# Performance work log

Hardware: AMD Instinct MI355X
Metric: run time of the kernel (lower is better)

The kernel has to match this reference:

```python
import jax, jax.numpy as jnp
import numpy as np
import math

_EPS = 1e-5          # _SAMPLING_EPS
_K_PER_CHUNK = 32    # _TOPK_K_PER_CHUNK
_MAX_CHUNK = 32768   # _TOPK_MAX_CHUNK_SIZE
B, V = 128, 128256


def setup_inputs() -> dict:
    key = jax.random.key(0)
    ks = jax.random.split(key, 10)
    logits = jax.random.normal(ks[0], (B, V), dtype=jnp.float32) * 4.0
    temperature = jax.random.uniform(ks[1], (B,), dtype=jnp.float32) * 1.5
    top_k = jax.random.randint(ks[2], (B,), 0, 100)  # 0 => top-k disabled
    top_p = 0.5 + 0.5 * jax.random.uniform(ks[3], (B,), dtype=jnp.float32)
    output_token_counts = jax.random.randint(ks[4], (B, V), 0, 3).astype(jnp.float32)
    prompt_token_mask = jax.random.randint(ks[5], (B, V), 0, 2).astype(bool)
    presence_penalties = jax.random.uniform(ks[6], (B,), dtype=jnp.float32)
    frequency_penalties = jax.random.uniform(ks[7], (B,), dtype=jnp.float32)
    repetition_penalties = 1.0 + 0.5 * jax.random.uniform(ks[8], (B,), dtype=jnp.float32)
    u = jax.random.uniform(ks[9], (B, V), dtype=jnp.float32, minval=1e-6, maxval=1.0)
    q_samples = -jnp.log(u)  # Exponential(1) noise, vLLM random_sample convention
    return dict(logits=logits, temperature=temperature, top_k=top_k, top_p=top_p,
                output_token_counts=output_token_counts, prompt_token_mask=prompt_token_mask,
                presence_penalties=presence_penalties, frequency_penalties=frequency_penalties,
                repetition_penalties=repetition_penalties, q_samples=q_samples)


def _apply_penalties(logits, counts, prompt_mask, presence, frequency, repetition):
    counts = counts.astype(logits.dtype)
    prompt_f = prompt_mask.astype(logits.dtype)
    occurred = counts - jnp.maximum(counts - 1.0, 0.0)            # 1 if count>0 else 0
    rep_union = occurred + prompt_f
    rep_mask = rep_union - jnp.maximum(rep_union - 1.0, 0.0)      # 1 if in prompt or output
    rep = repetition[:, None]
    pos = jnp.maximum(logits, 0.0)
    neg = jnp.minimum(logits, 0.0)
    penalized = pos / rep + neg * rep
    logits = logits + rep_mask * (penalized - logits)
    logits = logits - frequency[:, None] * counts - presence[:, None] * occurred
    return logits


def _chunked_topk(logits):
    # split vocab into <=32768 chunks, top-32 per chunk (multi-core ttnn.topk emulation)
    b, v = logits.shape
    num_chunks = math.ceil(v / _MAX_CHUNK)
    chunk_size = math.ceil(v / num_chunks)
    pad = num_chunks * chunk_size - v
    x = jnp.pad(logits, ((0, 0), (0, pad)), constant_values=-np.inf) if pad else logits
    x = x.reshape(b, num_chunks, chunk_size)
    vals, inds = jax.lax.top_k(x, _K_PER_CHUNK)                   # [b, nc, k]
    inds = inds + (jnp.arange(num_chunks, dtype=inds.dtype) * chunk_size)[None, :, None]
    return vals.reshape(b, -1), inds.reshape(b, -1)               # [b, nc*k]


def _filter_topk_topp(all_values, k, p, vocab_size):
    C = all_values.shape[-1]
    probs = jax.nn.softmax(all_values, axis=-1)
    probs_sort = jnp.sort(probs, axis=-1)                         # ascending
    # top-k on candidate set
    count_k = jnp.clip(C - k.astype(jnp.int32), 0, C - 1)[:, None]
    cutoff_k = jnp.take_along_axis(probs_sort, count_k, axis=-1)
    no_k = ((k <= 0) | (k >= vocab_size))[:, None]
    cutoff_k = jnp.where(no_k, -np.inf, cutoff_k)
    all_values = jnp.where(probs < cutoff_k, -np.inf, all_values)
    # top-p on candidate set
    cumprob = jnp.cumsum(probs_sort, axis=-1)
    mask = cumprob <= (1.0 - p)[:, None]
    mask = mask.at[:, -1].set(False)
    count_p = jnp.sum(mask, axis=-1, dtype=jnp.int32)[:, None]
    cutoff_p = jnp.take_along_axis(probs_sort, count_p, axis=-1)
    all_values = jnp.where(probs < cutoff_p, -np.inf, all_values)
    return all_values


def reference(logits, temperature, top_k, top_p, output_token_counts, prompt_token_mask,
              presence_penalties, frequency_penalties, repetition_penalties, q_samples):
    logits = logits.astype(jnp.float32)
    logits = _apply_penalties(logits, output_token_counts, prompt_token_mask,
                              presence_penalties, frequency_penalties, repetition_penalties)
    greedy = jnp.argmax(logits, axis=-1)                          # [B]
    temp_eff = jnp.where(temperature < _EPS, 1.0, temperature)
    logits_t = logits / temp_eff[:, None]
    vals, inds = _chunked_topk(logits_t)                          # [B, 128] each
    filtered = _filter_topk_topp(vals, top_k, top_p, logits.shape[-1])
    probs = jax.nn.softmax(filtered, axis=-1)                     # fp32 softmax on candidates
    q_red = jnp.take_along_axis(q_samples, inds, axis=1)
    local = jnp.argmax(probs / q_red, axis=-1)                    # exponential-noise sampling
    random_sampled = jnp.take_along_axis(inds, local[:, None], axis=1)[:, 0]
    sampled = jnp.where(temperature < _EPS, greedy, random_sampled.astype(greedy.dtype))
    return sampled[:, None], probs                                # sampled_token_ids [B,1]
```

## Files before the change

kernel.cpp:

```cpp
#include <hip/hip_runtime.h>
#include <math.h>

#define BATCH   128
#define VOCAB   128256
#define NCHUNK  4
#define CSIZE   32064
#define CVEC    (CSIZE / 4)
#define T1      1024
#define NBKT    2048
#define CAP     2048
#define KSEL    32
#define CWIDTH  (NCHUNK * KSEL)
#define T2      128
#define TAILTID 848

__device__ __forceinline__ unsigned fenc(float f) {
    unsigned u = __float_as_uint(f);
    return (u & 0x80000000u) ? ~u : (u | 0x80000000u);
}

__device__ __forceinline__ float penalize(float l, float cnt, float pf,
                                          float rep, float freq, float pres) {
    float occ   = __fsub_rn(cnt, fmaxf(__fsub_rn(cnt, 1.0f), 0.0f));
    float ru    = __fadd_rn(occ, pf);
    float rmask = __fsub_rn(ru, fmaxf(__fsub_rn(ru, 1.0f), 0.0f));
    float pos   = fmaxf(l, 0.0f);
    float neg   = fminf(l, 0.0f);
    float pen   = __fadd_rn(__fdiv_rn(pos, rep), __fmul_rn(neg, rep));
    float p     = __fadd_rn(l, __fmul_rn(rmask, __fsub_rn(pen, l)));
    p = __fsub_rn(p, __fmul_rn(freq, cnt));
    p = __fsub_rn(p, __fmul_rn(pres, occ));
    return p;
}

__device__ __forceinline__ unsigned ldmask(const void* pm, long base, int i, int mtype) {
    if (mtype == 0) {
        return ((const unsigned*)((const unsigned char*)pm + base))[i];
    } else if (mtype == 1) {
        int4 m = ((const int4*)((const int*)pm + base))[i];
        return (m.x ? 1u : 0u) | (m.y ? 0x100u : 0u) | (m.z ? 0x10000u : 0u) | (m.w ? 0x1000000u : 0u);
    } else {
        float4 f = ((const float4*)((const float*)pm + base))[i];
        return ((f.x != 0.f) ? 1u : 0u) | ((f.y != 0.f) ? 0x100u : 0u) |
               ((f.z != 0.f) ? 0x10000u : 0u) | ((f.w != 0.f) ? 0x1000000u : 0u);
    }
}

__global__ __launch_bounds__(T1, 4) void sampler_k1(
    const float* __restrict__ logits, const float* __restrict__ counts,
    const void* __restrict__ pmask,
    const float* __restrict__ temperature, const float* __restrict__ presence,
    const float* __restrict__ frequency, const float* __restrict__ repetition,
    float* __restrict__ g_topv, int* __restrict__ g_topi,
    float* __restrict__ g_gval, int* __restrict__ g_gidx)
{
    const int b   = blockIdx.x >> 2;
    const int c   = blockIdx.x & 3;
    const int tid = threadIdx.x;
    const long base = (long)b * VOCAB + (long)c * CSIZE;

    __shared__ unsigned hist[NBKT];
    __shared__ float    cv[CAP];
    __shared__ int      ci[CAP];
    __shared__ unsigned ccnt;
    __shared__ int      s_tb;
    __shared__ int      s_m0, s_mf;
    __shared__ float    wrv[16];
    __shared__ int      wri[16];

    for (int i = tid; i < NBKT; i += T1) hist[i] = 0;
    if (tid == 0) { ccnt = 0; s_m0 = 1; s_mf = 1; }
    __syncthreads();

    {
        const unsigned* w = (const unsigned*)pmask;
        int a01 = 1, af = 1;
        for (int i = tid; i < 4096; i += T1) {
            unsigned x = w[i];
            if (!(x == 0u || x == 1u)) a01 = 0;
            if (!(x == 0u || x == 0x3F800000u)) af = 0;
        }
        if (!a01) atomicAnd(&s_m0, 0);
        if (!af)  atomicAnd(&s_mf, 0);
    }
    __syncthreads();
    const int mtype = s_m0 ? 1 : (s_mf ? 2 : 0);

    const float temp = temperature[b];
    const float teff = (temp < 1e-5f) ? 1.0f : temp;
    const float pres = presence[b];
    const float freq = frequency[b];
    const float rep  = repetition[b];

    const float4* l4 = (const float4*)(logits + base);
    const float4* c4 = (const float4*)(counts + base);

    float gmax = -INFINITY;
    int   gidx = 0x7fffffff;

    const bool tail = tid < TAILTID;

    float4 v0, v1, v2, v3, v4, v5, v6, v7;
    v7.x = v7.y = v7.z = v7.w = 0.0f;

#define PROC1(Lv, Cv, Mv, Vv, I0) do {                                          \
        float p_;                                                               \
        p_ = penalize((Lv).x, (Cv).x, ((Mv) & 0x000000ffu) ? 1.0f : 0.0f,       \
                      rep, freq, pres);                                         \
        if (p_ > gmax) { gmax = p_; gidx = (I0) * 4 + 0; }                      \
        (Vv).x = __fdiv_rn(p_, teff);                                           \
        atomicAdd(&hist[fenc((Vv).x) >> 21], 1u);                               \
        p_ = penalize((Lv).y, (Cv).y, ((Mv) & 0x0000ff00u) ? 1.0f : 0.0f,       \
                      rep, freq, pres);                                         \
        if (p_ > gmax) { gmax = p_; gidx = (I0) * 4 + 1; }                      \
        (Vv).y = __fdiv_rn(p_, teff);                                           \
        atomicAdd(&hist[fenc((Vv).y) >> 21], 1u);                               \
        p_ = penalize((Lv).z, (Cv).z, ((Mv) & 0x00ff0000u) ? 1.0f : 0.0f,       \
                      rep, freq, pres);                                         \
        if (p_ > gmax) { gmax = p_; gidx = (I0) * 4 + 2; }                      \
        (Vv).z = __fdiv_rn(p_, teff);                                           \
        atomicAdd(&hist[fenc((Vv).z) >> 21], 1u);                               \
        p_ = penalize((Lv).w, (Cv).w, ((Mv) & 0xff000000u) ? 1.0f : 0.0f,       \
                      rep, freq, pres);                                         \
        if (p_ > gmax) { gmax = p_; gidx = (I0) * 4 + 3; }                      \
        (Vv).w = __fdiv_rn(p_, teff);                                           \
        atomicAdd(&hist[fenc((Vv).w) >> 21], 1u);                               \
    } while (0)

    {
        float4 L0 = l4[tid],          L1 = l4[tid + T1];
        float4 L2 = l4[tid + 2 * T1], L3 = l4[tid + 3 * T1];
        float4 C0 = c4[tid],          C1 = c4[tid + T1];
        float4 C2 = c4[tid + 2 * T1], C3 = c4[tid + 3 * T1];
        unsigned M0 = ldmask(pmask, base, tid,          mtype);
        unsigned M1 = ldmask(pmask, base, tid + T1,     mtype);
        unsigned M2 = ldmask(pmask, base, tid + 2 * T1, mtype);
        unsigned M3 = ldmask(pmask, base, tid + 3 * T1, mtype);
        PROC1(L0, C0, M0, v0, tid);
        PROC1(L1, C1, M1, v1, tid + T1);
        PROC1(L2, C2, M2, v2, tid + 2 * T1);
        PROC1(L3, C3, M3, v3, tid + 3 * T1);
    }
    {
        float4 L4 = l4[tid + 4 * T1], L5 = l4[tid + 5 * T1], L6 = l4[tid + 6 * T1];
        float4 C4 = c4[tid + 4 * T1], C5 = c4[tid + 5 * T1], C6 = c4[tid + 6 * T1];
        unsigned M4 = ldmask(pmask, base, tid + 4 * T1, mtype);
        unsigned M5 = ldmask(pmask, base, tid + 5 * T1, mtype);
        unsigned M6 = ldmask(pmask, base, tid + 6 * T1, mtype);
        float4 L7, C7; unsigned M7 = 0;
        if (tail) {
            L7 = l4[tid + 7 * T1];
            C7 = c4[tid + 7 * T1];
            M7 = ldmask(pmask, base, tid + 7 * T1, mtype);
        }
        PROC1(L4, C4, M4, v4, tid + 4 * T1);
        PROC1(L5, C5, M5, v5, tid + 5 * T1);
        PROC1(L6, C6, M6, v6, tid + 6 * T1);
        if (tail) PROC1(L7, C7, M7, v7, tid + 7 * T1);
    }
#undef PROC1

    for (int off = 32; off > 0; off >>= 1) {
        float ov = __shfl_down(gmax, off);
        int   oi = __shfl_down(gidx, off);
        if (ov > gmax || (ov == gmax && oi < gidx)) { gmax = ov; gidx = oi; }
    }
    if ((tid & 63) == 0) { wrv[tid >> 6] = gmax; wri[tid >> 6] = gidx; }
    __syncthreads();
    if (tid == 0) {
        float bv = wrv[0]; int bi = wri[0];
        for (int w2 = 1; w2 < 16; ++w2) {
            if (wrv[w2] > bv || (wrv[w2] == bv && wri[w2] < bi)) { bv = wrv[w2]; bi = wri[w2]; }
        }
        g_gval[blockIdx.x] = bv;
        g_gidx[blockIdx.x] = c * CSIZE + bi;
    }

    if (tid < 64) {
        const int gb = tid * 32;
        unsigned gs = 0;
#pragma unroll
        for (int k = 0; k < 32; ++k) gs += hist[gb + k];
        unsigned suf = gs;
#pragma unroll
        for (int off = 1; off < 64; off <<= 1) {
            unsigned o = __shfl_down(suf, off);
            if (tid + off < 64) suf += o;
        }
        unsigned sufn = __shfl_down(suf, 1);
        if (tid == 63) sufn = 0;
        if (suf >= (unsigned)KSEL && sufn < (unsigned)KSEL) {
            unsigned acc = sufn; int tb = gb;
            for (int q = gb + 31; q >= gb; --q) {
                acc += hist[q];
                if (acc >= (unsigned)KSEL) { tb = q; break; }
            }
            s_tb = tb;
        }
    }
    __syncthreads();
    const unsigned thr = ((unsigned)s_tb) << 21;

#define COLL(Vv, I0) do {                                                       \
        if (fenc((Vv).x) >= thr) {                                              \
            unsigned pos_ = atomicAdd(&ccnt, 1u);                               \
            if (pos_ < CAP) { cv[pos_] = (Vv).x; ci[pos_] = (I0) * 4 + 0; }     \
        }                                                                       \
        if (fenc((Vv).y) >= thr) {                                              \
            unsigned pos_ = atomicAdd(&ccnt, 1u);                               \
            if (pos_ < CAP) { cv[pos_] = (Vv).y; ci[pos_] = (I0) * 4 + 1; }     \
        }                                                                       \
        if (fenc((Vv).z) >= thr) {                                              \
            unsigned pos_ = atomicAdd(&ccnt, 1u);                               \
            if (pos_ < CAP) { cv[pos_] = (Vv).z; ci[pos_] = (I0) * 4 + 2; }     \
        }                                                                       \
        if (fenc((Vv).w) >= thr) {                                              \
            unsigned pos_ = atomicAdd(&ccnt, 1u);                               \
            if (pos_ < CAP) { cv[pos_] = (Vv).w; ci[pos_] = (I0) * 4 + 3; }     \
        }                                                                       \
    } while (0)

    COLL(v0, tid);
    COLL(v1, tid + T1);
    COLL(v2, tid + 2 * T1);
    COLL(v3, tid + 3 * T1);
    COLL(v4, tid + 4 * T1);
    COLL(v5, tid + 5 * T1);
    COLL(v6, tid + 6 * T1);
    if (tail) COLL(v7, tid + 7 * T1);
#undef COLL
    __syncthreads();

    unsigned m = ccnt;
    if (m > CAP) m = CAP;
    unsigned P = KSEL;
    while (P < m) P <<= 1;
    for (unsigned s = m + tid; s < P; s += T1) { cv[s] = -INFINITY; ci[s] = 0x7fffffff; }
    __syncthreads();

    for (unsigned k = 2; k <= P; k <<= 1) {
        for (unsigned j = k >> 1; j > 0; j >>= 1) {
            for (unsigned s = tid; s < P; s += T1) {
                unsigned x = s ^ j;
                if (x > s) {
                    float av = cv[s], bv = cv[x];
                    int   ai = ci[s], bi = ci[x];
                    bool xBetter = (bv > av) || (bv == av && bi < ai);
                    bool sBetter = (av > bv) || (av == bv && ai < bi);
                    bool doSwap  = ((s & k) == 0) ? xBetter : sBetter;
                    if (doSwap) { cv[s] = bv; cv[x] = av; ci[s] = bi; ci[x] = ai; }
                }
            }
            __syncthreads();
        }
    }

    if (tid < KSEL) {
        int o = blockIdx.x * KSEL + tid;
        g_topv[o] = cv[tid];
        g_topi[o] = c * CSIZE + ci[tid];
    }
}

__global__ __launch_bounds__(T2) void sampler_k2(
    const float* __restrict__ g_topv, const int* __restrict__ g_topi,
    const float* __restrict__ g_gval, const int* __restrict__ g_gidx,
    const float* __restrict__ temperature, const int* __restrict__ topk,
    const float* __restrict__ topp, const float* __restrict__ qs,
    float* __restrict__ out)
{
    const int b = blockIdx.x;
    const int j = threadIdx.x;

    __shared__ int   ix[T2];
    __shared__ float sv[T2];
    __shared__ float cum[T2];
    __shared__ float red[T2];
    __shared__ int   redi[T2];

    float val = g_topv[b * CWIDTH + j];
    int   idx = g_topi[b * CWIDTH + j];
    ix[j] = idx;

    red[j] = val; __syncthreads();
    for (int s = T2 / 2; s > 0; s >>= 1) {
        if (j < s) red[j] = fmaxf(red[j], red[j + s]);
        __syncthreads();
    }
    float m1 = red[0]; __syncthreads();
    float e = expf(__fsub_rn(val, m1));
    red[j] = e; __syncthreads();
    for (int s = T2 / 2; s > 0; s >>= 1) {
        if (j < s) red[j] = __fadd_rn(red[j], red[j + s]);
        __syncthreads();
    }
    float s1 = red[0]; __syncthreads();
    float prob = __fdiv_rn(e, s1);
    sv[j] = prob;
    __syncthreads();

    for (unsigned k = 2; k <= (unsigned)T2; k <<= 1) {
        for (unsigned jj = k >> 1; jj > 0; jj >>= 1) {
            unsigned x = (unsigned)j ^ jj;
            if (x > (unsigned)j) {
                float a = sv[j], bb = sv[x];
                bool sw = (((unsigned)j & k) == 0) ? (a > bb) : (a < bb);
                if (sw) { sv[j] = bb; sv[x] = a; }
            }
            __syncthreads();
        }
    }

    if (j == 0) {
        float a = 0.0f;
        for (int t = 0; t < T2; ++t) { a = __fadd_rn(a, sv[t]); cum[t] = a; }
    }
    __syncthreads();

    const int   k_row = topk[b];
    const float p_row = topp[b];
    int count_k = CWIDTH - k_row;
    count_k = min(max(count_k, 0), CWIDTH - 1);
    float cutoff_k = sv[count_k];
    if (k_row <= 0 || k_row >= VOCAB) cutoff_k = -INFINITY;

    float lim = __fsub_rn(1.0f, p_row);
    bool mk = (j < CWIDTH - 1) && (cum[j] <= lim);
    redi[j] = mk ? 1 : 0; __syncthreads();
    for (int s = T2 / 2; s > 0; s >>= 1) {
        if (j < s) redi[j] += redi[j + s];
        __syncthreads();
    }
    int count_p = redi[0]; __syncthreads();
    float cutoff_p = sv[count_p];

    float f = val;
    if (prob < cutoff_k) f = -INFINITY;
    if (prob < cutoff_p) f = -INFINITY;

    red[j] = f; __syncthreads();
    for (int s = T2 / 2; s > 0; s >>= 1) {
        if (j < s) red[j] = fmaxf(red[j], red[j + s]);
        __syncthreads();
    }
    float m2 = red[0]; __syncthreads();
    float e2 = (f == -INFINITY) ? 0.0f : expf(__fsub_rn(f, m2));
    red[j] = e2; __syncthreads();
    for (int s = T2 / 2; s > 0; s >>= 1) {
        if (j < s) red[j] = __fadd_rn(red[j], red[j + s]);
        __syncthreads();
    }
    float s2 = red[0]; __syncthreads();
    float pf = __fdiv_rn(e2, s2);
    out[BATCH + b * CWIDTH + j] = pf;

    float q = qs[(long)b * VOCAB + idx];
    float ratio = __fdiv_rn(pf, q);
    red[j] = ratio; redi[j] = j;
    __syncthreads();
    for (int s = T2 / 2; s > 0; s >>= 1) {
        if (j < s) {
            float o = red[j + s]; int oi = redi[j + s];
            if (o > red[j] || (o == red[j] && oi < redi[j])) { red[j] = o; redi[j] = oi; }
        }
        __syncthreads();
    }

    if (j == 0) {
        float bvv = g_gval[b * NCHUNK]; int bii = g_gidx[b * NCHUNK];
        for (int c2 = 1; c2 < NCHUNK; ++c2) {
            float w = g_gval[b * NCHUNK + c2]; int wi = g_gidx[b * NCHUNK + c2];
            if (w > bvv || (w == bvv && wi < bii)) { bvv = w; bii = wi; }
        }
        int token = ix[redi[0]];
        float tmp = temperature[b];
        int samp = (tmp < 1e-5f) ? bii : token;
        out[b] = (float)samp;
    }
}

extern "C" void kernel_launch(void* const* d_in, const int* in_sizes, int n_in,
                              void* d_out, int out_size, void* d_ws, size_t ws_size,
                              hipStream_t stream) {
    const float* logits = (const float*)d_in[0];
    const float* temp   = (const float*)d_in[1];
    const int*   topk   = (const int*)d_in[2];
    const float* topp   = (const float*)d_in[3];
    const float* counts = (const float*)d_in[4];
    const void*  pmask  = d_in[5];
    const float* pres   = (const float*)d_in[6];
    const float* freq   = (const float*)d_in[7];
    const float* rep    = (const float*)d_in[8];
    const float* qs     = (const float*)d_in[9];
    float* out = (float*)d_out;

    float* g_topv = (float*)d_ws;
    int*   g_topi = (int*)(g_topv + BATCH * CWIDTH);
    float* g_gval = (float*)(g_topi + BATCH * CWIDTH);
    int*   g_gidx = (int*)(g_gval + BATCH * NCHUNK);

    sampler_k1<<<BATCH * NCHUNK, T1, 0, stream>>>(
        logits, counts, pmask, temp, pres, freq, rep,
        g_topv, g_topi, g_gval, g_gidx);

    sampler_k2<<<BATCH, T2, 0, stream>>>(
        g_topv, g_topi, g_gval, g_gidx, temp, topk, topp, qs, out);
}
```

Baseline: 274.7 us.

## Histogram pre-temperature values and recompute candidates instead of holding them in registers

The first pass no longer keeps 32 temperature-scaled values per thread in registers. It builds the radix histogram on the penalized logits before division, which gives the same ordering because the effective temperature is positive, and records a per-float4-group maximum bucket. In the collect phase, only groups whose maximum bucket reaches the threshold reload logits, counts and mask, recompute the penalty, and divide by temperature for the values that pass. This cuts register pressure and removes most of the divisions. The costs are a second global read for the few surviving groups and dropping the min-blocks-per-CU launch bound.

```diff
diff --git a/kernel.cpp b/kernel.cpp
--- a/kernel.cpp
+++ b/kernel.cpp
@@ -46,7 +46,7 @@
     }
 }
 
-__global__ __launch_bounds__(T1, 4) void sampler_k1(
+__global__ __launch_bounds__(T1) void sampler_k1(
     const float* __restrict__ logits, const float* __restrict__ counts,
     const void* __restrict__ pmask,
     const float* __restrict__ temperature, const float* __restrict__ presence,
@@ -97,34 +97,32 @@
 
     float gmax = -INFINITY;
     int   gidx = 0x7fffffff;
-
     const bool tail = tid < TAILTID;
 
-    float4 v0, v1, v2, v3, v4, v5, v6, v7;
-    v7.x = v7.y = v7.z = v7.w = 0.0f;
-
-#define PROC1(Lv, Cv, Mv, Vv, I0) do {                                          \
-        float p_;                                                               \
+    unsigned gc0 = 0, gc1 = 0, gc2 = 0, gc3 = 0, gc4 = 0, gc5 = 0, gc6 = 0, gc7 = 0;
+
+#define PROC1(Lv, Cv, Mv, I0, GC) do {                                          \
+        float p_; unsigned bk_;                                                 \
         p_ = penalize((Lv).x, (Cv).x, ((Mv) & 0x000000ffu) ? 1.0f : 0.0f,       \
                       rep, freq, pres);                                         \
         if (p_ > gmax) { gmax = p_; gidx = (I0) * 4 + 0; }                      \
-        (Vv).x = __fdiv_rn(p_, teff);                                           \
-        atomicAdd(&hist[fenc((Vv).x) >> 21], 1u);                               \
+        bk_ = fenc(p_) >> 21; if (bk_ > (GC)) (GC) = bk_;                       \
+        atomicAdd(&hist[bk_], 1u);                                              \
         p_ = penalize((Lv).y, (Cv).y, ((Mv) & 0x0000ff00u) ? 1.0f : 0.0f,       \
                       rep, freq, pres);                                         \
         if (p_ > gmax) { gmax = p_; gidx = (I0) * 4 + 1; }                      \
-        (Vv).y = __fdiv_rn(p_, teff);                                           \
-        atomicAdd(&hist[fenc((Vv).y) >> 21], 1u);                               \
+        bk_ = fenc(p_) >> 21; if (bk_ > (GC)) (GC) = bk_;                       \
+        atomicAdd(&hist[bk_], 1u);                                              \
         p_ = penalize((Lv).z, (Cv).z, ((Mv) & 0x00ff0000u) ? 1.0f : 0.0f,       \
                       rep, freq, pres);                                         \
         if (p_ > gmax) { gmax = p_; gidx = (I0) * 4 + 2; }                      \
-        (Vv).z = __fdiv_rn(p_, teff);                                           \
-        atomicAdd(&hist[fenc((Vv).z) >> 21], 1u);                               \
+        bk_ = fenc(p_) >> 21; if (bk_ > (GC)) (GC) = bk_;                       \
+        atomicAdd(&hist[bk_], 1u);                                              \
         p_ = penalize((Lv).w, (Cv).w, ((Mv) & 0xff000000u) ? 1.0f : 0.0f,       \
                       rep, freq, pres);                                         \
         if (p_ > gmax) { gmax = p_; gidx = (I0) * 4 + 3; }                      \
-        (Vv).w = __fdiv_rn(p_, teff);                                           \
-        atomicAdd(&hist[fenc((Vv).w) >> 21], 1u);                               \
+        bk_ = fenc(p_) >> 21; if (bk_ > (GC)) (GC) = bk_;                       \
+        atomicAdd(&hist[bk_], 1u);                                              \
     } while (0)
 
     {
@@ -136,10 +134,10 @@
         unsigned M1 = ldmask(pmask, base, tid + T1,     mtype);
         unsigned M2 = ldmask(pmask, base, tid + 2 * T1, mtype);
         unsigned M3 = ldmask(pmask, base, tid + 3 * T1, mtype);
-        PROC1(L0, C0, M0, v0, tid);
-        PROC1(L1, C1, M1, v1, tid + T1);
-        PROC1(L2, C2, M2, v2, tid + 2 * T1);
-        PROC1(L3, C3, M3, v3, tid + 3 * T1);
+        PROC1(L0, C0, M0, tid,          gc0);
+        PROC1(L1, C1, M1, tid + T1,     gc1);
+        PROC1(L2, C2, M2, tid + 2 * T1, gc2);
+        PROC1(L3, C3, M3, tid + 3 * T1, gc3);
     }
     {
         float4 L4 = l4[tid + 4 * T1], L5 = l4[tid + 5 * T1], L6 = l4[tid + 6 * T1];
@@ -147,16 +145,15 @@
         unsigned M4 = ldmask(pmask, base, tid + 4 * T1, mtype);
         unsigned M5 = ldmask(pmask, base, tid + 5 * T1, mtype);
         unsigned M6 = ldmask(pmask, base, tid + 6 * T1, mtype);
-        float4 L7, C7; unsigned M7 = 0;
+        PROC1(L4, C4, M4, tid + 4 * T1, gc4);
+        PROC1(L5, C5, M5, tid + 5 * T1, gc5);
+        PROC1(L6, C6, M6, tid + 6 * T1, gc6);
         if (tail) {
-            L7 = l4[tid + 7 * T1];
-            C7 = c4[tid + 7 * T1];
-            M7 = ldmask(pmask, base, tid + 7 * T1, mtype);
-        }
-        PROC1(L4, C4, M4, v4, tid + 4 * T1);
-        PROC1(L5, C5, M5, v5, tid + 5 * T1);
-        PROC1(L6, C6, M6, v6, tid + 6 * T1);
-        if (tail) PROC1(L7, C7, M7, v7, tid + 7 * T1);
+            float4 L7 = l4[tid + 7 * T1];
+            float4 C7 = c4[tid + 7 * T1];
+            unsigned M7 = ldmask(pmask, base, tid + 7 * T1, mtype);
+            PROC1(L7, C7, M7, tid + 7 * T1, gc7);
+        }
     }
 #undef PROC1
 
@@ -199,36 +196,56 @@
         }
     }
     __syncthreads();
-    const unsigned thr = ((unsigned)s_tb) << 21;
-
-#define COLL(Vv, I0) do {                                                       \
-        if (fenc((Vv).x) >= thr) {                                              \
-            unsigned pos_ = atomicAdd(&ccnt, 1u);                               \
-            if (pos_ < CAP) { cv[pos_] = (Vv).x; ci[pos_] = (I0) * 4 + 0; }     \
-        }                                                                       \
-        if (fenc((Vv).y) >= thr) {                                              \
-            unsigned pos_ = atomicAdd(&ccnt, 1u);                               \
-            if (pos_ < CAP) { cv[pos_] = (Vv).y; ci[pos_] = (I0) * 4 + 1; }     \
-        }                                                                       \
-        if (fenc((Vv).z) >= thr) {                                              \
-            unsigned pos_ = atomicAdd(&ccnt, 1u);                               \
-            if (pos_ < CAP) { cv[pos_] = (Vv).z; ci[pos_] = (I0) * 4 + 2; }     \
-        }                                                                       \
-        if (fenc((Vv).w) >= thr) {                                              \
-            unsigned pos_ = atomicAdd(&ccnt, 1u);                               \
-            if (pos_ < CAP) { cv[pos_] = (Vv).w; ci[pos_] = (I0) * 4 + 3; }     \
+    const unsigned tbv = (unsigned)s_tb;
+    const unsigned thr = tbv << 21;
+
+#define COLLG(GC, K) do {                                                       \
+        if ((GC) >= tbv) {                                                      \
+            const int g_ = tid + (K) * T1;                                      \
+            float4 L_ = l4[g_];                                                 \
+            float4 C_ = c4[g_];                                                 \
+            unsigned M_ = ldmask(pmask, base, g_, mtype);                       \
+            float p_;                                                           \
+            p_ = penalize(L_.x, C_.x, (M_ & 0x000000ffu) ? 1.0f : 0.0f,         \
+                          rep, freq, pres);                                     \
+            if (fenc(p_) >= thr) {                                              \
+                unsigned pos_ = atomicAdd(&ccnt, 1u);                           \
+                if (pos_ < CAP) { cv[pos_] = __fdiv_rn(p_, teff);               \
+                                  ci[pos_] = g_ * 4 + 0; }                      \
+            }                                                                   \
+            p_ = penalize(L_.y, C_.y, (M_ & 0x0000ff00u) ? 1.0f : 0.0f,         \
+                          rep, freq, pres);                                     \
+            if (fenc(p_) >= thr) {                                              \
+                unsigned pos_ = atomicAdd(&ccnt, 1u);                           \
+                if (pos_ < CAP) { cv[pos_] = __fdiv_rn(p_, teff);               \
+                                  ci[pos_] = g_ * 4 + 1; }                      \
+            }                                                                   \
+            p_ = penalize(L_.z, C_.z, (M_ & 0x00ff0000u) ? 1.0f : 0.0f,         \
+                          rep, freq, pres);                                     \
+            if (fenc(p_) >= thr) {                                              \
+                unsigned pos_ = atomicAdd(&ccnt, 1u);                           \
+                if (pos_ < CAP) { cv[pos_] = __fdiv_rn(p_, teff);               \
+                                  ci[pos_] = g_ * 4 + 2; }                      \
+            }                                                                   \
+            p_ = penalize(L_.w, C_.w, (M_ & 0xff000000u) ? 1.0f : 0.0f,         \
+                          rep, freq, pres);                                     \
+            if (fenc(p_) >= thr) {                                              \
+                unsigned pos_ = atomicAdd(&ccnt, 1u);                           \
+                if (pos_ < CAP) { cv[pos_] = __fdiv_rn(p_, teff);               \
+                                  ci[pos_] = g_ * 4 + 3; }                      \
+            }                                                                   \
         }                                                                       \
     } while (0)
 
-    COLL(v0, tid);
-    COLL(v1, tid + T1);
-    COLL(v2, tid + 2 * T1);
-    COLL(v3, tid + 3 * T1);
-    COLL(v4, tid + 4 * T1);
-    COLL(v5, tid + 5 * T1);
-    COLL(v6, tid + 6 * T1);
-    if (tail) COLL(v7, tid + 7 * T1);
-#undef COLL
+    COLLG(gc0, 0);
+    COLLG(gc1, 1);
+    COLLG(gc2, 2);
+    COLLG(gc3, 3);
+    COLLG(gc4, 4);
+    COLLG(gc5, 5);
+    COLLG(gc6, 6);
+    if (tail) COLLG(gc7, 7);
+#undef COLLG
     __syncthreads();
 
     unsigned m = ccnt;
```

Result: slower. 283.8 us (+3.3%).
